# Optimization experiments

Measured on AMD Instinct MI355X. Metric: run time of the kernel, lower is better.

## Reference

```python
import jax, jax.numpy as jnp
import numpy as np

K = 3
K2 = K * K
EPS = 1e-5


def conv2d(x, w, stride=1, pad=1):
    return jax.lax.conv_general_dilated(
        x, w, (stride, stride), [(pad, pad), (pad, pad)],
        dimension_numbers=("NCHW", "OIHW", "NCHW"))


def bilinear_sample(x, py, px):
    """x: [B,C,H,W]; py,px: [B,Ho,Wo,K2] float sample coords.
    Zero padding outside bounds (torchvision deform_conv2d semantics).
    Returns [B,C,Ho,Wo,K2]."""
    B, C, H, W = x.shape
    Ho, Wo = py.shape[1], py.shape[2]
    y0 = jnp.floor(py)
    x0 = jnp.floor(px)
    wy1 = py - y0
    wx1 = px - x0
    x_flat = x.reshape(B, C, H * W)

    def gather(yi, xi):
        valid = (yi >= 0) & (yi < H) & (xi >= 0) & (xi < W)
        yc = jnp.clip(yi, 0, H - 1).astype(jnp.int32)
        xc = jnp.clip(xi, 0, W - 1).astype(jnp.int32)
        idx = (yc * W + xc).reshape(B, 1, -1)          # [B,1,N]
        v = jnp.take_along_axis(x_flat, idx, axis=2)   # [B,C,N]
        return v * valid.reshape(B, 1, -1).astype(x.dtype)

    w00 = ((1 - wy1) * (1 - wx1)).reshape(B, 1, -1)
    w01 = ((1 - wy1) * wx1).reshape(B, 1, -1)
    w10 = (wy1 * (1 - wx1)).reshape(B, 1, -1)
    w11 = (wy1 * wx1).reshape(B, 1, -1)
    val = (w00 * gather(y0, x0) + w01 * gather(y0, x0 + 1)
           + w10 * gather(y0 + 1, x0) + w11 * gather(y0 + 1, x0 + 1))
    return val.reshape(B, C, Ho, Wo, K2)


def deform_conv_bn_relu(x, d, offset_w, conv_w, gamma, beta):
    # offset branch: 3x3 conv on d, clamp to [-1,1]
    offset = jnp.clip(conv2d(d, offset_w, 1, 1), -1.0, 1.0)  # [B,2*K2,H,W]
    B, Cin, H, W = x.shape
    Cout = conv_w.shape[0]
    off = offset.reshape(B, K2, 2, H, W)
    dy = off[:, :, 0].transpose(0, 2, 3, 1)  # [B,H,W,K2]
    dx = off[:, :, 1].transpose(0, 2, 3, 1)
    kh = (jnp.arange(K2) // K).astype(jnp.float32)
    kw = (jnp.arange(K2) % K).astype(jnp.float32)
    # sample coords: out pixel + kernel tap - padding + learned offset
    py = (jnp.arange(H, dtype=jnp.float32)[None, :, None, None] - 1.0
          + kh[None, None, None, :] + dy)
    px = (jnp.arange(W, dtype=jnp.float32)[None, None, :, None] - 1.0
          + kw[None, None, None, :] + dx)
    sampled = bilinear_sample(x, py, px)  # [B,Cin,H,W,K2]
    out = jnp.einsum('bchwk,ock->bohw', sampled,
                     conv_w.reshape(Cout, Cin, K2))
    # BatchNorm2d (training forward: biased batch stats) + ReLU
    mean = out.mean(axis=(0, 2, 3))
    var = out.var(axis=(0, 2, 3))
    inv = gamma / jnp.sqrt(var + EPS)
    out = (out - mean[None, :, None, None]) * inv[None, :, None, None] \
        + beta[None, :, None, None]
    out = jax.nn.relu(out)
    return out, offset


def setup_inputs() -> dict:
    key = jax.random.key(0)
    k1, k2, k3, k4 = jax.random.split(key, 4)
    B, C, H, W = 4, 64, 160, 160
    Cout, offC = 64, 64
    x = jax.random.normal(k1, (B, C, H, W), dtype=jnp.float32)
    d = jax.random.normal(k2, (B, offC, H, W), dtype=jnp.float32)
    # torch zero-inits offset_conv; use small random weights so the
    # bilinear gather path is actually exercised with fractional offsets
    offset_w = jax.random.normal(k3, (2 * K2, offC, K, K), dtype=jnp.float32) * 0.01
    conv_w = jax.random.normal(k4, (Cout, C, K, K), dtype=jnp.float32) * (1.0 / np.sqrt(C * K2))
    gamma = jnp.ones((Cout,), dtype=jnp.float32)
    beta = jnp.zeros((Cout,), dtype=jnp.float32)
    return {"x": x, "d": d, "offset_w": offset_w, "conv_w": conv_w,
            "gamma": gamma, "beta": beta}


def reference(x, d, offset_w, conv_w, gamma, beta):
    return deform_conv_bn_relu(x, d, offset_w, conv_w, gamma, beta)
```

## Files before the change

kernel.cpp:

```cpp
#include <hip/hip_runtime.h>
#include <hip/hip_bf16.h>

#define BB 4
#define HH 160
#define WW 160
#define HWD (HH * WW)
#define OUT_ELEMS (BB * 64 * HWD)
#define OFF_ELEMS (BB * 18 * HWD)
#define EPSBN 1e-5f
#define CHSTRIDE (8 * HWD)
#define NSLOT 256

typedef __attribute__((ext_vector_type(8))) short bf16x8;
typedef __attribute__((ext_vector_type(4))) float f32x4;

__device__ inline unsigned pack2bf(float a, float b) {
  __hip_bfloat162 h2 = __float22bfloat162_rn(float2{a, b});
  unsigned u;
  __builtin_memcpy(&u, &h2, 4);
  return u;
}
__device__ inline unsigned short bf16bits(float a) {
  __hip_bfloat16 h = __float2bfloat16(a);
  unsigned short u;
  __builtin_memcpy(&u, &h, 2);
  return u;
}

__device__ inline void tile_map(int blk, int& b, int& ty0, int& tx0) {
  int t = (blk & 7) * 200 + (blk >> 3);
  b = t / 400;
  int r = t % 400;
  ty0 = (r / 10) * 4;
  tx0 = (r % 10) * 16;
}

__global__ void prep_kernel(const float* __restrict__ cw,
                            const float* __restrict__ ow,
                            unsigned short* __restrict__ Bp,
                            unsigned short* __restrict__ B2p,
                            float* __restrict__ part) {
  int i = blockIdx.x * 256 + threadIdx.x;
  if (i < 32768) part[i] = 0.f;
  if (i < 49152) {
    int j = i & 7, l = (i >> 3) & 63, rest = i >> 9;
    int ki = rest % 24, nt = rest / 24;
    int kp = ki * 32 + ((l >> 4) << 3) + j;
    int chunk = kp / 96, kq = kp % 96;
    int t = kq >> 3, c = kq & 7;
    int n = nt * 16 + (l & 15);
    float v = (t < 9) ? cw[n * 576 + (chunk * 8 + c) * 9 + t] : 0.f;
    Bp[i] = bf16bits(v);
  }
  if (i < 24576) {
    int j = i & 7, l = (i >> 3) & 63, rest = i >> 9;
    int ki = rest % 24, nt = rest / 24;
    int kp = ki * 32 + ((l >> 4) << 3) + j;
    int chunk = kp / 96, kq = kp % 96;
    int t = kq >> 3, c = kq & 7;
    int n = nt * 16 + (l & 15);
    float v = (t < 9 && n < 18) ? ow[n * 576 + (chunk * 8 + c) * 9 + t] : 0.f;
    B2p[i] = bf16bits(v);
  }
}

__global__ __launch_bounds__(256) void offconv_kernel(
    const float* __restrict__ d, const bf16x8* __restrict__ B2p,
    float* __restrict__ off_out) {
  int b, ty0, tx0;
  tile_map(blockIdx.x, b, ty0, tx0);
  const int tid = threadIdx.x;
  const int wv = tid >> 6, lane = tid & 63;
  const int lo = lane >> 4, li = lane & 15;
  const int px = li, py = wv;

  __shared__ float p2[108 * 12];
  __shared__ bf16x8 Af[768];

  int poff[3];
  bool tre[3];
#pragma unroll
  for (int kk = 0; kk < 3; ++kk) {
    int t = kk * 4 + lo;
    tre[kk] = (t < 9);
    poff[kk] = tre[kk] ? ((py + t / 3) * 18 + px + t % 3) : 0;
  }

  int goff[4], laddr[4];
  bool gok[4];
#pragma unroll
  for (int i = 0; i < 4; ++i) {
    int l = tid + i * 256;
    int c = l / 108, rc = l % 108, r = rc / 18, col = rc % 18;
    int gy = ty0 - 1 + r, gx = tx0 - 1 + col;
    gok[i] = (l < 864) && gy >= 0 && gy < HH && gx >= 0 && gx < WW;
    goff[i] = ((b * 64 + c) * HH + gy) * WW + gx;
    laddr[i] = rc * 12 + c;
  }
  float g[4];
#pragma unroll
  for (int i = 0; i < 4; ++i) g[i] = gok[i] ? d[goff[i]] : 0.f;

  f32x4 acc0{0.f, 0.f, 0.f, 0.f}, acc1{0.f, 0.f, 0.f, 0.f};
  const int nt = wv >> 1, mh = wv & 1;

  for (int chunk = 0; chunk < 8; ++chunk) {
    bf16x8 bw0 = B2p[((nt * 24 + chunk * 3 + 0) << 6) + lane];
    bf16x8 bw1 = B2p[((nt * 24 + chunk * 3 + 1) << 6) + lane];
    bf16x8 bw2 = B2p[((nt * 24 + chunk * 3 + 2) << 6) + lane];
#pragma unroll
    for (int i = 0; i < 4; ++i) {
      int l = tid + i * 256;
      if (l < 864) p2[laddr[i]] = g[i];
    }
    __syncthreads();
    int nco = ((chunk < 7) ? (chunk + 1) : 7) * CHSTRIDE;
#pragma unroll
    for (int i = 0; i < 4; ++i) g[i] = gok[i] ? d[goff[i] + nco] : 0.f;
#pragma unroll
    for (int kk = 0; kk < 3; ++kk) {
      union { bf16x8 v; unsigned u[4]; } a;
      if (tre[kk]) {
        const float* q = p2 + poff[kk] * 12;
        float4 c0 = *(const float4*)(q);
        float4 c1 = *(const float4*)(q + 4);
        a.u[0] = pack2bf(c0.x, c0.y);
        a.u[1] = pack2bf(c0.z, c0.w);
        a.u[2] = pack2bf(c1.x, c1.y);
        a.u[3] = pack2bf(c1.z, c1.w);
      } else {
        a.u[0] = a.u[1] = a.u[2] = a.u[3] = 0u;
      }
      Af[((wv * 3 + kk) << 6) + lane] = a.v;
    }
    __syncthreads();
#pragma unroll
    for (int kk = 0; kk < 3; ++kk) {
      bf16x8 bw = (kk == 0) ? bw0 : (kk == 1) ? bw1 : bw2;
      acc0 = __builtin_amdgcn_mfma_f32_16x16x32_bf16(
          Af[(((mh * 2) * 3 + kk) << 6) + lane], bw, acc0, 0, 0, 0);
      acc1 = __builtin_amdgcn_mfma_f32_16x16x32_bf16(
          Af[(((mh * 2 + 1) * 3 + kk) << 6) + lane], bw, acc1, 0, 0, 0);
    }
  }
  const int n = nt * 16 + li;
  if (n < 18) {
#pragma unroll
    for (int f = 0; f < 2; ++f) {
      int mf = mh * 2 + f;
      f32x4 a = f ? acc1 : acc0;
      float* po = off_out + ((b * 18 + n) * HH + ty0 + mf) * WW + tx0 + lo * 4;
      float4 v;
      v.x = fminf(1.f, fmaxf(-1.f, a[0]));
      v.y = fminf(1.f, fmaxf(-1.f, a[1]));
      v.z = fminf(1.f, fmaxf(-1.f, a[2]));
      v.w = fminf(1.f, fmaxf(-1.f, a[3]));
      *(float4*)po = v;
    }
  }
}

__global__ __launch_bounds__(256) void dconv_kernel(
    const float* __restrict__ x, const float* __restrict__ offs,
    const bf16x8* __restrict__ Bp, float* __restrict__ out,
    float* __restrict__ part) {
  int b, ty0, tx0;
  tile_map(blockIdx.x, b, ty0, tx0);
  const int tid = threadIdx.x;
  const int wv = tid >> 6, lane = tid & 63;
  const int lo = lane >> 4, li = lane & 15;
  const int px = li, py = wv;
  const int h = ty0 + py, w = tx0 + px;

  __shared__ float patch[189 * 12];
  __shared__ bf16x8 Af[768];

  int bs[3];
  float W00[3], W01[3], W10[3], W11[3];
  bool tre[3];
#pragma unroll
  for (int kk = 0; kk < 3; ++kk) {
    int t = kk * 4 + lo;
    tre[kk] = (t < 9);
    if (tre[kk]) {
      float dy = offs[((b * 18 + 2 * t) * HH + h) * WW + w];
      float dx = offs[((b * 18 + 2 * t + 1) * HH + h) * WW + w];
      float pyf = (float)(h - 1 + t / 3) + dy;
      float pxf = (float)(w - 1 + t % 3) + dx;
      float y0 = floorf(pyf), x0 = floorf(pxf);
      float wy = pyf - y0, wx = pxf - x0;
      bs[kk] = ((int)y0 - (ty0 - 2)) * 21 + ((int)x0 - (tx0 - 2));
      W00[kk] = (1.f - wy) * (1.f - wx);
      W01[kk] = (1.f - wy) * wx;
      W10[kk] = wy * (1.f - wx);
      W11[kk] = wy * wx;
    } else {
      bs[kk] = 0;
      W00[kk] = W01[kk] = W10[kk] = W11[kk] = 0.f;
    }
  }

  int goff[6], laddr[6];
  bool gok[6];
#pragma unroll
  for (int i = 0; i < 6; ++i) {
    int l = tid + i * 256;
    int c = l / 189, rc = l % 189, r = rc / 21, col = rc % 21;
    int gy = ty0 - 2 + r, gx = tx0 - 2 + col;
    gok[i] = (l < 1512) && gy >= 0 && gy < HH && gx >= 0 && gx < WW;
    goff[i] = ((b * 64 + c) * HH + gy) * WW + gx;
    laddr[i] = rc * 12 + c;
  }
  float g[6];
#pragma unroll
  for (int i = 0; i < 6; ++i) g[i] = gok[i] ? x[goff[i]] : 0.f;

  f32x4 acc[4];
#pragma unroll
  for (int i = 0; i < 4; ++i) acc[i] = f32x4{0.f, 0.f, 0.f, 0.f};
  const int nt = wv;

  for (int chunk = 0; chunk < 8; ++chunk) {
    bf16x8 bw0 = Bp[((nt * 24 + chunk * 3 + 0) << 6) + lane];
    bf16x8 bw1 = Bp[((nt * 24 + chunk * 3 + 1) << 6) + lane];
    bf16x8 bw2 = Bp[((nt * 24 + chunk * 3 + 2) << 6) + lane];
#pragma unroll
    for (int i = 0; i < 6; ++i) {
      int l = tid + i * 256;
      if (l < 1512) patch[laddr[i]] = g[i];
    }
    __syncthreads();
    int nco = ((chunk < 7) ? (chunk + 1) : 7) * CHSTRIDE;
#pragma unroll
    for (int i = 0; i < 6; ++i) g[i] = gok[i] ? x[goff[i] + nco] : 0.f;
#pragma unroll
    for (int kk = 0; kk < 3; ++kk) {
      union { bf16x8 v; unsigned u[4]; } a;
      if (tre[kk]) {
        const float* q = patch + bs[kk] * 12;
        float4 p00a = *(const float4*)(q);
        float4 p00b = *(const float4*)(q + 4);
        float4 p01a = *(const float4*)(q + 12);
        float4 p01b = *(const float4*)(q + 16);
        float4 p10a = *(const float4*)(q + 252);
        float4 p10b = *(const float4*)(q + 256);
        float4 p11a = *(const float4*)(q + 264);
        float4 p11b = *(const float4*)(q + 268);
        float w0 = W00[kk], w1 = W01[kk], w2 = W10[kk], w3 = W11[kk];
        float v0 = fmaf(w3, p11a.x, fmaf(w2, p10a.x, fmaf(w1, p01a.x, w0 * p00a.x)));
        float v1 = fmaf(w3, p11a.y, fmaf(w2, p10a.y, fmaf(w1, p01a.y, w0 * p00a.y)));
        float v2 = fmaf(w3, p11a.z, fmaf(w2, p10a.z, fmaf(w1, p01a.z, w0 * p00a.z)));
        float v3 = fmaf(w3, p11a.w, fmaf(w2, p10a.w, fmaf(w1, p01a.w, w0 * p00a.w)));
        float v4 = fmaf(w3, p11b.x, fmaf(w2, p10b.x, fmaf(w1, p01b.x, w0 * p00b.x)));
        float v5 = fmaf(w3, p11b.y, fmaf(w2, p10b.y, fmaf(w1, p01b.y, w0 * p00b.y)));
        float v6 = fmaf(w3, p11b.z, fmaf(w2, p10b.z, fmaf(w1, p01b.z, w0 * p00b.z)));
        float v7 = fmaf(w3, p11b.w, fmaf(w2, p10b.w, fmaf(w1, p01b.w, w0 * p00b.w)));
        a.u[0] = pack2bf(v0, v1);
        a.u[1] = pack2bf(v2, v3);
        a.u[2] = pack2bf(v4, v5);
        a.u[3] = pack2bf(v6, v7);
      } else {
        a.u[0] = a.u[1] = a.u[2] = a.u[3] = 0u;
      }
      Af[((wv * 3 + kk) << 6) + lane] = a.v;
    }
    __syncthreads();
#pragma unroll
    for (int kk = 0; kk < 3; ++kk) {
      bf16x8 bw = (kk == 0) ? bw0 : (kk == 1) ? bw1 : bw2;
#pragma unroll
      for (int mf = 0; mf < 4; ++mf)
        acc[mf] = __builtin_amdgcn_mfma_f32_16x16x32_bf16(
            Af[((mf * 3 + kk) << 6) + lane], bw, acc[mf], 0, 0, 0);
    }
  }
  const int n = nt * 16 + li;
  float s = 0.f, s2 = 0.f;
#pragma unroll
  for (int mf = 0; mf < 4; ++mf) {
    float* po = out + ((b * 64 + n) * HH + ty0 + mf) * WW + tx0 + lo * 4;
    *(float4*)po = make_float4(acc[mf][0], acc[mf][1], acc[mf][2], acc[mf][3]);
#pragma unroll
    for (int r = 0; r < 4; ++r) {
      float v = acc[mf][r];
      s += v;
      s2 = fmaf(v, v, s2);
    }
  }
  s += __shfl_xor(s, 16);  s += __shfl_xor(s, 32);
  s2 += __shfl_xor(s2, 16); s2 += __shfl_xor(s2, 32);
  if (lo == 0) {
    int slot = blockIdx.x & (NSLOT - 1);
    atomicAdd(&part[n * NSLOT + slot], s);
    atomicAdd(&part[(64 + n) * NSLOT + slot], s2);
  }
}

__global__ __launch_bounds__(256) void reduce_kernel(
    const float* __restrict__ part, double* __restrict__ sums) {
  const int j = blockIdx.x;
  __shared__ double sh[256];
  sh[threadIdx.x] = (double)part[j * NSLOT + threadIdx.x];
  __syncthreads();
  for (int t = 128; t > 0; t >>= 1) {
    if (threadIdx.x < t) sh[threadIdx.x] += sh[threadIdx.x + t];
    __syncthreads();
  }
  if (threadIdx.x == 0) sums[j] = sh[0];
}

__global__ __launch_bounds__(256) void bnapply_kernel(
    float* __restrict__ out, const double* __restrict__ sums,
    const float* __restrict__ gamma, const float* __restrict__ beta) {
  const int i = blockIdx.x * 256 + threadIdx.x;
  if (i >= OUT_ELEMS / 4) return;
  const int o = (i / (HWD / 4)) & 63;
  const float n_inv = 1.0f / (float)(BB * HWD);
  float mean = (float)sums[o] * n_inv;
  float var = (float)sums[64 + o] * n_inv - mean * mean;
  float inv = gamma[o] * rsqrtf(var + EPSBN);
  float bt = beta[o];
  float4 v = ((float4*)out)[i];
  v.x = fmaxf(0.f, (v.x - mean) * inv + bt);
  v.y = fmaxf(0.f, (v.y - mean) * inv + bt);
  v.z = fmaxf(0.f, (v.z - mean) * inv + bt);
  v.w = fmaxf(0.f, (v.w - mean) * inv + bt);
  ((float4*)out)[i] = v;
}

extern "C" void kernel_launch(void* const* d_in, const int* in_sizes, int n_in,
                              void* d_out, int out_size, void* d_ws, size_t ws_size,
                              hipStream_t stream) {
  const float* x = (const float*)d_in[0];
  const float* d = (const float*)d_in[1];
  const float* ow = (const float*)d_in[2];
  const float* cw = (const float*)d_in[3];
  const float* gamma = (const float*)d_in[4];
  const float* beta = (const float*)d_in[5];

  float* out = (float*)d_out;
  float* off_out = out + OUT_ELEMS;

  double* sums = (double*)d_ws;
  unsigned short* Bp = (unsigned short*)((char*)d_ws + 1024);
  unsigned short* B2p = Bp + 49152;
  float* part = (float*)(B2p + 24576);

  prep_kernel<<<192, 256, 0, stream>>>(cw, ow, Bp, B2p, part);

  offconv_kernel<<<1600, 256, 0, stream>>>(d, (const bf16x8*)B2p, off_out);
  dconv_kernel<<<1600, 256, 0, stream>>>(x, off_out, (const bf16x8*)Bp, out,
                                         part);

  reduce_kernel<<<128, 256, 0, stream>>>(part, sums);
  bnapply_kernel<<<(OUT_ELEMS / 4 + 255) / 256, 256, 0, stream>>>(
      out, sums, gamma, beta);
}
```

Measured before the change: 164.4 us.

## Fuse offset conv into deformable conv kernel with fp16 patch staging

Merges the offset-conv and deform-conv kernels into one per-tile kernel. Offsets are passed through shared memory instead of being re-read from global memory, and one launch is removed. Input patches are packed to fp16 pairs in LDS, bilinear interpolation uses half2 FMAs, and the MFMAs switch from bf16 to f16, which halves LDS traffic and the VALU work for the patches. The trade-off is lower interpolation precision in fp16, a risk of fp16 range overflow, and a longer serial kernel per block with more shared memory in use.

```diff
diff --git a/kernel.cpp b/kernel.cpp
--- a/kernel.cpp
+++ b/kernel.cpp
@@ -1,30 +1,27 @@
 #include <hip/hip_runtime.h>
 #include <hip/hip_bf16.h>
+#include <hip/hip_fp16.h>
 
 #define BB 4
 #define HH 160
 #define WW 160
 #define HWD (HH * WW)
 #define OUT_ELEMS (BB * 64 * HWD)
-#define OFF_ELEMS (BB * 18 * HWD)
 #define EPSBN 1e-5f
 #define CHSTRIDE (8 * HWD)
 #define NSLOT 256
 
-typedef __attribute__((ext_vector_type(8))) short bf16x8;
+typedef _Float16 f16x8 __attribute__((ext_vector_type(8)));
 typedef __attribute__((ext_vector_type(4))) float f32x4;
 
-__device__ inline unsigned pack2bf(float a, float b) {
-  __hip_bfloat162 h2 = __float22bfloat162_rn(float2{a, b});
-  unsigned u;
-  __builtin_memcpy(&u, &h2, 4);
-  return u;
-}
-__device__ inline unsigned short bf16bits(float a) {
-  __hip_bfloat16 h = __float2bfloat16(a);
+__device__ inline unsigned short f16bits(float a) {
+  _Float16 h = (_Float16)a;
   unsigned short u;
   __builtin_memcpy(&u, &h, 2);
   return u;
+}
+__device__ inline unsigned packh2(float a, float b) {
+  return (unsigned)f16bits(a) | ((unsigned)f16bits(b) << 16);
 }
 
 __device__ inline void tile_map(int blk, int& b, int& ty0, int& tx0) {
@@ -50,7 +47,7 @@
     int t = kq >> 3, c = kq & 7;
     int n = nt * 16 + (l & 15);
     float v = (t < 9) ? cw[n * 576 + (chunk * 8 + c) * 9 + t] : 0.f;
-    Bp[i] = bf16bits(v);
+    Bp[i] = f16bits(v);
   }
   if (i < 24576) {
     int j = i & 7, l = (i >> 3) & 63, rest = i >> 9;
@@ -60,205 +57,180 @@
     int t = kq >> 3, c = kq & 7;
     int n = nt * 16 + (l & 15);
     float v = (t < 9 && n < 18) ? ow[n * 576 + (chunk * 8 + c) * 9 + t] : 0.f;
-    B2p[i] = bf16bits(v);
-  }
-}
-
-__global__ __launch_bounds__(256) void offconv_kernel(
-    const float* __restrict__ d, const bf16x8* __restrict__ B2p,
-    float* __restrict__ off_out) {
-  int b, ty0, tx0;
-  tile_map(blockIdx.x, b, ty0, tx0);
-  const int tid = threadIdx.x;
-  const int wv = tid >> 6, lane = tid & 63;
-  const int lo = lane >> 4, li = lane & 15;
-  const int px = li, py = wv;
-
-  __shared__ float p2[108 * 12];
-  __shared__ bf16x8 Af[768];
-
-  int poff[3];
-  bool tre[3];
-#pragma unroll
-  for (int kk = 0; kk < 3; ++kk) {
-    int t = kk * 4 + lo;
-    tre[kk] = (t < 9);
-    poff[kk] = tre[kk] ? ((py + t / 3) * 18 + px + t % 3) : 0;
-  }
-
-  int goff[4], laddr[4];
-  bool gok[4];
-#pragma unroll
-  for (int i = 0; i < 4; ++i) {
-    int l = tid + i * 256;
-    int c = l / 108, rc = l % 108, r = rc / 18, col = rc % 18;
-    int gy = ty0 - 1 + r, gx = tx0 - 1 + col;
-    gok[i] = (l < 864) && gy >= 0 && gy < HH && gx >= 0 && gx < WW;
-    goff[i] = ((b * 64 + c) * HH + gy) * WW + gx;
-    laddr[i] = rc * 12 + c;
-  }
-  float g[4];
-#pragma unroll
-  for (int i = 0; i < 4; ++i) g[i] = gok[i] ? d[goff[i]] : 0.f;
-
-  f32x4 acc0{0.f, 0.f, 0.f, 0.f}, acc1{0.f, 0.f, 0.f, 0.f};
-  const int nt = wv >> 1, mh = wv & 1;
-
-  for (int chunk = 0; chunk < 8; ++chunk) {
-    bf16x8 bw0 = B2p[((nt * 24 + chunk * 3 + 0) << 6) + lane];
-    bf16x8 bw1 = B2p[((nt * 24 + chunk * 3 + 1) << 6) + lane];
-    bf16x8 bw2 = B2p[((nt * 24 + chunk * 3 + 2) << 6) + lane];
-#pragma unroll
-    for (int i = 0; i < 4; ++i) {
-      int l = tid + i * 256;
-      if (l < 864) p2[laddr[i]] = g[i];
-    }
-    __syncthreads();
-    int nco = ((chunk < 7) ? (chunk + 1) : 7) * CHSTRIDE;
-#pragma unroll
-    for (int i = 0; i < 4; ++i) g[i] = gok[i] ? d[goff[i] + nco] : 0.f;
-#pragma unroll
-    for (int kk = 0; kk < 3; ++kk) {
-      union { bf16x8 v; unsigned u[4]; } a;
-      if (tre[kk]) {
-        const float* q = p2 + poff[kk] * 12;
-        float4 c0 = *(const float4*)(q);
-        float4 c1 = *(const float4*)(q + 4);
-        a.u[0] = pack2bf(c0.x, c0.y);
-        a.u[1] = pack2bf(c0.z, c0.w);
-        a.u[2] = pack2bf(c1.x, c1.y);
-        a.u[3] = pack2bf(c1.z, c1.w);
-      } else {
-        a.u[0] = a.u[1] = a.u[2] = a.u[3] = 0u;
-      }
-      Af[((wv * 3 + kk) << 6) + lane] = a.v;
-    }
-    __syncthreads();
-#pragma unroll
-    for (int kk = 0; kk < 3; ++kk) {
-      bf16x8 bw = (kk == 0) ? bw0 : (kk == 1) ? bw1 : bw2;
-      acc0 = __builtin_amdgcn_mfma_f32_16x16x32_bf16(
-          Af[(((mh * 2) * 3 + kk) << 6) + lane], bw, acc0, 0, 0, 0);
-      acc1 = __builtin_amdgcn_mfma_f32_16x16x32_bf16(
-          Af[(((mh * 2 + 1) * 3 + kk) << 6) + lane], bw, acc1, 0, 0, 0);
-    }
-  }
-  const int n = nt * 16 + li;
-  if (n < 18) {
-#pragma unroll
-    for (int f = 0; f < 2; ++f) {
-      int mf = mh * 2 + f;
-      f32x4 a = f ? acc1 : acc0;
-      float* po = off_out + ((b * 18 + n) * HH + ty0 + mf) * WW + tx0 + lo * 4;
-      float4 v;
-      v.x = fminf(1.f, fmaxf(-1.f, a[0]));
-      v.y = fminf(1.f, fmaxf(-1.f, a[1]));
-      v.z = fminf(1.f, fmaxf(-1.f, a[2]));
-      v.w = fminf(1.f, fmaxf(-1.f, a[3]));
-      *(float4*)po = v;
-    }
-  }
-}
-
-__global__ __launch_bounds__(256) void dconv_kernel(
-    const float* __restrict__ x, const float* __restrict__ offs,
-    const bf16x8* __restrict__ Bp, float* __restrict__ out,
+    B2p[i] = f16bits(v);
+  }
+}
+
+__global__ __launch_bounds__(256) void fused_kernel(
+    const float* __restrict__ x, const float* __restrict__ d,
+    const f16x8* __restrict__ Bp, const f16x8* __restrict__ B2p,
+    float* __restrict__ out, float* __restrict__ off_out,
     float* __restrict__ part) {
   int b, ty0, tx0;
   tile_map(blockIdx.x, b, ty0, tx0);
   const int tid = threadIdx.x;
   const int wv = tid >> 6, lane = tid & 63;
   const int lo = lane >> 4, li = lane & 15;
-  const int px = li, py = wv;
-  const int h = ty0 + py, w = tx0 + px;
-
-  __shared__ float patch[189 * 12];
-  __shared__ bf16x8 Af[768];
-
+
+  __shared__ __align__(16) unsigned patch2[756];
+  __shared__ f16x8 Af[768];
+  __shared__ float offbuf[64 * 19];
+
+  int gdo[2], gdl[2];
+  bool gdk[2];
+#pragma unroll
+  for (int i = 0; i < 2; ++i) {
+    int l = tid + i * 256;
+    int p = l % 108, c2 = l / 108;
+    int r = p / 18, col = p % 18;
+    int gy = ty0 - 1 + r, gx = tx0 - 1 + col;
+    gdk[i] = (l < 432) && gy >= 0 && gy < HH && gx >= 0 && gx < WW;
+    gdo[i] = ((b * 64 + 2 * c2) * HH + gy) * WW + gx;
+    gdl[i] = p * 4 + c2;
+  }
+  unsigned gd[2];
+#pragma unroll
+  for (int i = 0; i < 2; ++i)
+    gd[i] = gdk[i] ? packh2(d[gdo[i]], d[gdo[i] + HWD]) : 0u;
+
+  int gxo[3], gxl[3];
+  bool gxk[3];
+#pragma unroll
+  for (int i = 0; i < 3; ++i) {
+    int l = tid + i * 256;
+    int p = l % 189, c2 = l / 189;
+    int r = p / 21, col = p % 21;
+    int gy = ty0 - 2 + r, gx2 = tx0 - 2 + col;
+    gxk[i] = (l < 756) && gy >= 0 && gy < HH && gx2 >= 0 && gx2 < WW;
+    gxo[i] = ((b * 64 + 2 * c2) * HH + gy) * WW + gx2;
+    gxl[i] = p * 4 + c2;
+  }
+  unsigned gx[3];
+
+  f32x4 acc0{0.f, 0.f, 0.f, 0.f}, acc1{0.f, 0.f, 0.f, 0.f};
+  const int nt = wv >> 1, mh = wv & 1;
+  int poffA[3];
+#pragma unroll
+  for (int kk = 0; kk < 3; ++kk) {
+    int t = kk * 4 + lo;
+    if (t > 8) t = 8;
+    poffA[kk] = ((t / 3) * 18 + t % 3 + li) * 4;
+  }
+
+  for (int chunk = 0; chunk < 8; ++chunk) {
+    f16x8 bw0 = B2p[((nt * 24 + chunk * 3 + 0) << 6) + lane];
+    f16x8 bw1 = B2p[((nt * 24 + chunk * 3 + 1) << 6) + lane];
+    f16x8 bw2 = B2p[((nt * 24 + chunk * 3 + 2) << 6) + lane];
+#pragma unroll
+    for (int i = 0; i < 2; ++i)
+      if (tid + i * 256 < 432) patch2[gdl[i]] = gd[i];
+    __syncthreads();
+    if (chunk < 7) {
+      int nco = (chunk + 1) * CHSTRIDE;
+#pragma unroll
+      for (int i = 0; i < 2; ++i)
+        gd[i] = gdk[i] ? packh2(d[gdo[i] + nco], d[gdo[i] + nco + HWD]) : 0u;
+    } else {
+#pragma unroll
+      for (int i = 0; i < 3; ++i)
+        gx[i] = gxk[i] ? packh2(x[gxo[i]], x[gxo[i] + HWD]) : 0u;
+    }
+#pragma unroll
+    for (int kk = 0; kk < 3; ++kk) {
+      f16x8 bw = (kk == 0) ? bw0 : (kk == 1) ? bw1 : bw2;
+      const f16x8* a0 = (const f16x8*)(patch2 + poffA[kk] + (mh * 2) * 72);
+      const f16x8* a1 = (const f16x8*)(patch2 + poffA[kk] + (mh * 2 + 1) * 72);
+      acc0 = __builtin_amdgcn_mfma_f32_16x16x32_f16(*a0, bw, acc0, 0, 0, 0);
+      acc1 = __builtin_amdgcn_mfma_f32_16x16x32_f16(*a1, bw, acc1, 0, 0, 0);
+    }
+    __syncthreads();
+  }
+
+  const int nA = nt * 16 + li;
+  if (nA < 18) {
+#pragma unroll
+    for (int f = 0; f < 2; ++f) {
+      int mf = mh * 2 + f;
+      f32x4 a = f ? acc1 : acc0;
+      float4 v;
+      v.x = fminf(1.f, fmaxf(-1.f, a[0]));
+      v.y = fminf(1.f, fmaxf(-1.f, a[1]));
+      v.z = fminf(1.f, fmaxf(-1.f, a[2]));
+      v.w = fminf(1.f, fmaxf(-1.f, a[3]));
+      offbuf[(mf * 16 + lo * 4 + 0) * 19 + nA] = v.x;
+      offbuf[(mf * 16 + lo * 4 + 1) * 19 + nA] = v.y;
+      offbuf[(mf * 16 + lo * 4 + 2) * 19 + nA] = v.z;
+      offbuf[(mf * 16 + lo * 4 + 3) * 19 + nA] = v.w;
+      *(float4*)(off_out + ((b * 18 + nA) * HH + ty0 + mf) * WW + tx0 +
+                 lo * 4) = v;
+    }
+  }
+  __syncthreads();
+
+  const int h = ty0 + wv, w = tx0 + li;
+  const int m_pix = wv * 16 + li;
   int bs[3];
-  float W00[3], W01[3], W10[3], W11[3];
   bool tre[3];
+  __half2 w00h[3], w01h[3], w10h[3], w11h[3];
 #pragma unroll
   for (int kk = 0; kk < 3; ++kk) {
     int t = kk * 4 + lo;
     tre[kk] = (t < 9);
     if (tre[kk]) {
-      float dy = offs[((b * 18 + 2 * t) * HH + h) * WW + w];
-      float dx = offs[((b * 18 + 2 * t + 1) * HH + h) * WW + w];
+      float dy = offbuf[m_pix * 19 + 2 * t];
+      float dx = offbuf[m_pix * 19 + 2 * t + 1];
       float pyf = (float)(h - 1 + t / 3) + dy;
       float pxf = (float)(w - 1 + t % 3) + dx;
       float y0 = floorf(pyf), x0 = floorf(pxf);
       float wy = pyf - y0, wx = pxf - x0;
-      bs[kk] = ((int)y0 - (ty0 - 2)) * 21 + ((int)x0 - (tx0 - 2));
-      W00[kk] = (1.f - wy) * (1.f - wx);
-      W01[kk] = (1.f - wy) * wx;
-      W10[kk] = wy * (1.f - wx);
-      W11[kk] = wy * wx;
+      bs[kk] = (((int)y0 - (ty0 - 2)) * 21 + ((int)x0 - (tx0 - 2))) * 4;
+      w00h[kk] = __float2half2_rn((1.f - wy) * (1.f - wx));
+      w01h[kk] = __float2half2_rn((1.f - wy) * wx);
+      w10h[kk] = __float2half2_rn(wy * (1.f - wx));
+      w11h[kk] = __float2half2_rn(wy * wx);
     } else {
       bs[kk] = 0;
-      W00[kk] = W01[kk] = W10[kk] = W11[kk] = 0.f;
-    }
-  }
-
-  int goff[6], laddr[6];
-  bool gok[6];
-#pragma unroll
-  for (int i = 0; i < 6; ++i) {
-    int l = tid + i * 256;
-    int c = l / 189, rc = l % 189, r = rc / 21, col = rc % 21;
-    int gy = ty0 - 2 + r, gx = tx0 - 2 + col;
-    gok[i] = (l < 1512) && gy >= 0 && gy < HH && gx >= 0 && gx < WW;
-    goff[i] = ((b * 64 + c) * HH + gy) * WW + gx;
-    laddr[i] = rc * 12 + c;
-  }
-  float g[6];
-#pragma unroll
-  for (int i = 0; i < 6; ++i) g[i] = gok[i] ? x[goff[i]] : 0.f;
+      w00h[kk] = w01h[kk] = w10h[kk] = w11h[kk] = __float2half2_rn(0.f);
+    }
+  }
 
   f32x4 acc[4];
 #pragma unroll
   for (int i = 0; i < 4; ++i) acc[i] = f32x4{0.f, 0.f, 0.f, 0.f};
-  const int nt = wv;
+
+  union u4h { uint4 q; __half2 hh[4]; unsigned u[4]; f16x8 v; };
 
   for (int chunk = 0; chunk < 8; ++chunk) {
-    bf16x8 bw0 = Bp[((nt * 24 + chunk * 3 + 0) << 6) + lane];
-    bf16x8 bw1 = Bp[((nt * 24 + chunk * 3 + 1) << 6) + lane];
-    bf16x8 bw2 = Bp[((nt * 24 + chunk * 3 + 2) << 6) + lane];
-#pragma unroll
-    for (int i = 0; i < 6; ++i) {
-      int l = tid + i * 256;
-      if (l < 1512) patch[laddr[i]] = g[i];
-    }
-    __syncthreads();
-    int nco = ((chunk < 7) ? (chunk + 1) : 7) * CHSTRIDE;
-#pragma unroll
-    for (int i = 0; i < 6; ++i) g[i] = gok[i] ? x[goff[i] + nco] : 0.f;
+    f16x8 bw0 = Bp[((wv * 24 + chunk * 3 + 0) << 6) + lane];
+    f16x8 bw1 = Bp[((wv * 24 + chunk * 3 + 1) << 6) + lane];
+    f16x8 bw2 = Bp[((wv * 24 + chunk * 3 + 2) << 6) + lane];
+#pragma unroll
+    for (int i = 0; i < 3; ++i)
+      if (tid + i * 256 < 756) patch2[gxl[i]] = gx[i];
+    __syncthreads();
+    if (chunk < 7) {
+      int nco = (chunk + 1) * CHSTRIDE;
+#pragma unroll
+      for (int i = 0; i < 3; ++i)
+        gx[i] = gxk[i] ? packh2(x[gxo[i] + nco], x[gxo[i] + nco + HWD]) : 0u;
+    }
 #pragma unroll
     for (int kk = 0; kk < 3; ++kk) {
-      union { bf16x8 v; unsigned u[4]; } a;
+      u4h a;
       if (tre[kk]) {
-        const float* q = patch + bs[kk] * 12;
-        float4 p00a = *(const float4*)(q);
-        float4 p00b = *(const float4*)(q + 4);
-        float4 p01a = *(const float4*)(q + 12);
-        float4 p01b = *(const float4*)(q + 16);
-        float4 p10a = *(const float4*)(q + 252);
-        float4 p10b = *(const float4*)(q + 256);
-        float4 p11a = *(const float4*)(q + 264);
-        float4 p11b = *(const float4*)(q + 268);
-        float w0 = W00[kk], w1 = W01[kk], w2 = W10[kk], w3 = W11[kk];
-        float v0 = fmaf(w3, p11a.x, fmaf(w2, p10a.x, fmaf(w1, p01a.x, w0 * p00a.x)));
-        float v1 = fmaf(w3, p11a.y, fmaf(w2, p10a.y, fmaf(w1, p01a.y, w0 * p00a.y)));
-        float v2 = fmaf(w3, p11a.z, fmaf(w2, p10a.z, fmaf(w1, p01a.z, w0 * p00a.z)));
-        float v3 = fmaf(w3, p11a.w, fmaf(w2, p10a.w, fmaf(w1, p01a.w, w0 * p00a.w)));
-        float v4 = fmaf(w3, p11b.x, fmaf(w2, p10b.x, fmaf(w1, p01b.x, w0 * p00b.x)));
-        float v5 = fmaf(w3, p11b.y, fmaf(w2, p10b.y, fmaf(w1, p01b.y, w0 * p00b.y)));
-        float v6 = fmaf(w3, p11b.z, fmaf(w2, p10b.z, fmaf(w1, p01b.z, w0 * p00b.z)));
-        float v7 = fmaf(w3, p11b.w, fmaf(w2, p10b.w, fmaf(w1, p01b.w, w0 * p00b.w)));
-        a.u[0] = pack2bf(v0, v1);
-        a.u[1] = pack2bf(v2, v3);
-        a.u[2] = pack2bf(v4, v5);
-        a.u[3] = pack2bf(v6, v7);
+        u4h q00, q01, q10, q11;
+        q00.q = *(const uint4*)(patch2 + bs[kk]);
+        q01.q = *(const uint4*)(patch2 + bs[kk] + 4);
+        q10.q = *(const uint4*)(patch2 + bs[kk] + 84);
+        q11.q = *(const uint4*)(patch2 + bs[kk] + 88);
+#pragma unroll
+        for (int j = 0; j < 4; ++j) {
+          __half2 v = __hmul2(w00h[kk], q00.hh[j]);
+          v = __hfma2(w01h[kk], q01.hh[j], v);
+          v = __hfma2(w10h[kk], q10.hh[j], v);
+          v = __hfma2(w11h[kk], q11.hh[j], v);
+          a.hh[j] = v;
+        }
       } else {
         a.u[0] = a.u[1] = a.u[2] = a.u[3] = 0u;
       }
@@ -267,14 +239,15 @@
     __syncthreads();
 #pragma unroll
     for (int kk = 0; kk < 3; ++kk) {
-      bf16x8 bw = (kk == 0) ? bw0 : (kk == 1) ? bw1 : bw2;
+      f16x8 bw = (kk == 0) ? bw0 : (kk == 1) ? bw1 : bw2;
 #pragma unroll
       for (int mf = 0; mf < 4; ++mf)
-        acc[mf] = __builtin_amdgcn_mfma_f32_16x16x32_bf16(
+        acc[mf] = __builtin_amdgcn_mfma_f32_16x16x32_f16(
             Af[((mf * 3 + kk) << 6) + lane], bw, acc[mf], 0, 0, 0);
     }
   }
-  const int n = nt * 16 + li;
+
+  const int n = wv * 16 + li;
   float s = 0.f, s2 = 0.f;
 #pragma unroll
   for (int mf = 0; mf < 4; ++mf) {
@@ -287,8 +260,10 @@
       s2 = fmaf(v, v, s2);
     }
   }
-  s += __shfl_xor(s, 16);  s += __shfl_xor(s, 32);
-  s2 += __shfl_xor(s2, 16); s2 += __shfl_xor(s2, 32);
+  s += __shfl_xor(s, 16);
+  s += __shfl_xor(s, 32);
+  s2 += __shfl_xor(s2, 16);
+  s2 += __shfl_xor(s2, 32);
   if (lo == 0) {
     int slot = blockIdx.x & (NSLOT - 1);
     atomicAdd(&part[n * NSLOT + slot], s);
@@ -348,9 +323,8 @@
 
   prep_kernel<<<192, 256, 0, stream>>>(cw, ow, Bp, B2p, part);
 
-  offconv_kernel<<<1600, 256, 0, stream>>>(d, (const bf16x8*)B2p, off_out);
-  dconv_kernel<<<1600, 256, 0, stream>>>(x, off_out, (const bf16x8*)Bp, out,
-                                         part);
+  fused_kernel<<<1600, 256, 0, stream>>>(
+      x, d, (const f16x8*)Bp, (const f16x8*)B2p, out, off_out, part);
 
   reduce_kernel<<<128, 256, 0, stream>>>(part, sums);
   bnapply_kernel<<<(OUT_ELEMS / 4 + 255) / 256, 256, 0, stream>>>(
```

New measurement: 178.3 us. 1.08x slower.
